# Kernel optimization log

Measured on AMD Instinct MI355X. Metric: run time of the kernel, lower is better.

## Reference

```python
import jax, jax.numpy as jnp
import numpy as np

N = 200000
C_IN, C_OUT = 32, 64
D, H, W = 32, 512, 512
EPS = 1e-5


def _build_nbrs(lin, d, h, w, offsets):
    # lin: sorted unique linear voxel indices [N]; returns [N, K] int64 (sentinel=N)
    n = lin.shape[0]
    cols = []
    for dz, dy, dx in offsets:
        nd, nh, nw = d + dz, h + dy, w + dx
        valid = (nd >= 0) & (nd < D) & (nh >= 0) & (nh < H) & (nw >= 0) & (nw < W)
        nlin = nd * (H * W) + nh * W + nw
        pos = np.searchsorted(lin, nlin)
        posc = np.clip(pos, 0, n - 1)
        found = valid & (pos < n) & (lin[posc] == nlin)
        cols.append(np.where(found, posc, n))
    return np.stack(cols, axis=1).astype(np.int64)


def setup_inputs() -> dict:
    rng = np.random.default_rng(0)
    lin = np.sort(rng.choice(D * H * W, size=N, replace=False))
    d = lin // (H * W)
    h = (lin // W) % H
    w = lin % W
    # (1,3,3) kernel, padding (0,1,1): dz=0
    off133 = [(0, dy, dx) for dy in (-1, 0, 1) for dx in (-1, 0, 1)]
    # (3,1,3) kernel, padding (1,0,1): dy=0
    off313 = [(dz, 0, dx) for dz in (-1, 0, 1) for dx in (-1, 0, 1)]
    nbr133 = jnp.asarray(_build_nbrs(lin, d, h, w, off133))
    nbr313 = jnp.asarray(_build_nbrs(lin, d, h, w, off313))

    key = jax.random.key(0)
    ks = jax.random.split(key, 5)
    feats = jax.random.normal(ks[0], (N, C_IN), dtype=jnp.float32)
    s_in = 1.0 / np.sqrt(9 * C_IN)
    s_out = 1.0 / np.sqrt(9 * C_OUT)
    W1 = jax.random.normal(ks[1], (9, C_IN, C_OUT), dtype=jnp.float32) * s_in
    W2 = jax.random.normal(ks[2], (9, C_OUT, C_OUT), dtype=jnp.float32) * s_out
    W3 = jax.random.normal(ks[3], (9, C_IN, C_OUT), dtype=jnp.float32) * s_in
    W4 = jax.random.normal(ks[4], (9, C_OUT, C_OUT), dtype=jnp.float32) * s_out
    ones = jnp.ones((C_OUT,), jnp.float32)
    zeros = jnp.zeros((C_OUT,), jnp.float32)
    return dict(feats=feats, nbr133=nbr133, nbr313=nbr313,
                W1=W1, W2=W2, W3=W3, W4=W4,
                g0=ones, b0=zeros, g02=ones, b02=zeros,
                g1=ones, b1=zeros, g2=ones, b2=zeros)


def _subm_conv(x, nbr, Wk):
    # x: [N, Cin], nbr: [N, K] with sentinel N -> zero row, Wk: [K, Cin, Cout]
    xp = jnp.concatenate([x, jnp.zeros((1, x.shape[1]), x.dtype)], axis=0)
    g = xp[nbr]  # [N, K, Cin] gather
    return jnp.einsum('nkc,kcd->nd', g, Wk)


def _bn(x, gamma, beta):
    # training-mode BatchNorm1d: batch stats over N (biased variance)
    m = x.mean(axis=0)
    v = x.var(axis=0)
    return gamma * (x - m) * jax.lax.rsqrt(v + EPS) + beta


def _lrelu(x):
    return jax.nn.leaky_relu(x, 0.01)


def reference(feats, nbr133, nbr313, W1, W2, W3, W4,
              g0, b0, g02, b02, g1, b1, g2, b2):
    shortcut = _subm_conv(feats, nbr133, W1)
    shortcut = _bn(_lrelu(shortcut), g0, b0)
    shortcut = _subm_conv(shortcut, nbr313, W2)
    shortcut = _bn(_lrelu(shortcut), g02, b02)

    resA = _subm_conv(feats, nbr313, W3)
    resA = _bn(_lrelu(resA), g1, b1)
    resA = _subm_conv(resA, nbr133, W4)
    resA = _bn(_lrelu(resA), g2, b2)
    return resA + shortcut
```

## Files before the change

### kernel.cpp

```cpp
#include <hip/hip_runtime.h>
#include <hip/hip_bf16.h>


typedef __attribute__((ext_vector_type(8))) short bf16x8;
typedef __attribute__((ext_vector_type(4))) float f32x4;
typedef unsigned long long ull;

#define EPSF 1e-5f
#define REP8 0x0101010101010101ull

__device__ __forceinline__ unsigned short f2bf(float f) {
    union { __hip_bfloat16 h; unsigned short u; } cv;
    cv.h = __float2bfloat16(f);
    return cv.u;
}
__device__ __forceinline__ unsigned pkbf(float lo, float hi) {
    return (unsigned)f2bf(lo) | ((unsigned)f2bf(hi) << 16);
}

__global__ void prep_kernel(const float* __restrict__ W1, const float* __restrict__ W3,
                            unsigned short* __restrict__ Wb1, unsigned short* __restrict__ Wb3)
{
    int i = blockIdx.x * 256 + threadIdx.x;
    if (i >= 2 * 9 * 2048) return;
    const float* W = i < 9 * 2048 ? W1 : W3;
    unsigned short* Wb = i < 9 * 2048 ? Wb1 : Wb3;
    int pp = i < 9 * 2048 ? i : i - 9 * 2048;
    int k = pp >> 11, rest = pp & 2047;
    int t = (rest >> 9) & 3, lane = (rest >> 3) & 63, j = rest & 7;
    int c = (lane >> 4) * 8 + j;
    int d = t * 16 + (lane & 15);
    Wb[pp] = f2bf(W[(size_t)(k * 32 + c) * 64 + d]);
}

__global__ __launch_bounds__(256, 4)
void conv13_kernel(const float* __restrict__ x,
                   const int* __restrict__ nbrA, const int* __restrict__ nbrB,
                   const unsigned short* __restrict__ WbA,
                   const unsigned short* __restrict__ WbB,
                   unsigned short* __restrict__ yA, unsigned short* __restrict__ yB,
                   float* __restrict__ part,
                   int n_vox)
{
    const int lane = threadIdx.x & 63;
    const int wave = threadIdx.x >> 6;
    __shared__ __align__(16) char smem[4][4352];
    char* my = smem[wave];
    const int c15 = lane & 15, g16 = lane >> 4;
    const int j7 = lane & 7, kk = j7 + (j7 >= 4 ? 1 : 0), vv = lane >> 3;
    const int v16 = blockIdx.x * 64 + wave * 16;

    const size_t r0 = (size_t)(v16 + vv) * 9 + kk;
    const size_t r1 = (size_t)(v16 + 8 + vv) * 9 + kk;
    int pA0 = nbrA[r0], pA1 = nbrA[r1];
    int pB0 = nbrB[r0], pB1 = nbrB[r1];

    const float* xr = x + (size_t)(v16 + c15) * 32 + g16 * 8;
    float4 x0 = *reinterpret_cast<const float4*>(xr);
    float4 x1 = *reinterpret_cast<const float4*>(xr + 4);

    bf16x8 bA[4], bB[4];
    #pragma unroll
    for (int t = 0; t < 4; ++t) {
        bA[t] = *reinterpret_cast<const bf16x8*>(WbA + (size_t)((4*4+t)*64 + lane) * 8);
        bB[t] = *reinterpret_cast<const bf16x8*>(WbB + (size_t)((4*4+t)*64 + lane) * 8);
    }
    bf16x8 af;
    af[0]=(short)f2bf(x0.x); af[1]=(short)f2bf(x0.y); af[2]=(short)f2bf(x0.z); af[3]=(short)f2bf(x0.w);
    af[4]=(short)f2bf(x1.x); af[5]=(short)f2bf(x1.y); af[6]=(short)f2bf(x1.z); af[7]=(short)f2bf(x1.w);

    f32x4 accA[4], accB[4];
    #pragma unroll
    for (int t = 0; t < 4; ++t) { f32x4 z = {0.f,0.f,0.f,0.f}; accA[t] = z; accB[t] = z; }
    #pragma unroll
    for (int t = 0; t < 4; ++t) {
        accA[t] = __builtin_amdgcn_mfma_f32_16x16x32_bf16(af, bA[t], accA[t], 0, 0, 0);
        accB[t] = __builtin_amdgcn_mfma_f32_16x16x32_bf16(af, bB[t], accB[t], 0, 0, 0);
    }

    ull mA0 = __ballot(pA0 < n_vox), mA1 = __ballot(pA1 < n_vox);
    ull mB0 = __ballot(pB0 < n_vox), mB1 = __ballot(pB1 < n_vox);
    const int nhA = __popcll(mA0) + __popcll(mA1);
    const int nhB = __popcll(mB0) + __popcll(mB1);

    auto walksel = [&](ull M, int preg, int slot, int base, int& sel) {
        while (M) {
            int b = __builtin_ctzll(M); M &= M - 1;
            int src = __shfl(preg, b);
            sel = (c15 == slot - base) ? src : sel;
            ++slot;
        }
        return slot;
    };
    auto gatherfrag = [&](int sel) {
        const float* hr = x + (size_t)sel * 32 + g16 * 8;
        float4 f0 = *reinterpret_cast<const float4*>(hr);
        float4 f1 = *reinterpret_cast<const float4*>(hr + 4);
        bf16x8 h;
        h[0]=(short)f2bf(f0.x); h[1]=(short)f2bf(f0.y); h[2]=(short)f2bf(f0.z); h[3]=(short)f2bf(f0.w);
        h[4]=(short)f2bf(f1.x); h[5]=(short)f2bf(f1.y); h[6]=(short)f2bf(f1.z); h[7]=(short)f2bf(f1.w);
        return h;
    };
    auto kloop = [&](ull m0, ull m1, bf16x8 h, const unsigned short* Wb,
                     f32x4* acc, int base) {
        const int pref = __popcll(m0);
        for (int tap = 0; tap < 8; ++tap) {
            ull TM = REP8 << tap;
            ull k0 = m0 & TM, k1 = m1 & TM;
            if (!(k0 | k1)) continue;
            int k = tap + (tap >= 4 ? 1 : 0);
            bf16x8 bk[4];
            #pragma unroll
            for (int t = 0; t < 4; ++t)
                bk[t] = *reinterpret_cast<const bf16x8*>(Wb + (size_t)((k*4+t)*64 + lane) * 8);
            f32x4 ch[4];
            #pragma unroll
            for (int t = 0; t < 4; ++t) { f32x4 z = {0.f,0.f,0.f,0.f}; ch[t] = z; }
            #pragma unroll
            for (int t = 0; t < 4; ++t)
                ch[t] = __builtin_amdgcn_mfma_f32_16x16x32_bf16(h, bk[t], ch[t], 0, 0, 0);
            auto inj = [&](ull M, ull msrc, int spref, int vbase) {
                while (M) {
                    int b = __builtin_ctzll(M); M &= M - 1;
                    int slot = spref + __popcll(msrc & ((1ull << b) - 1ull));
                    int rs = slot - base;
                    if (rs < 0 || rs >= 16) continue;
                    int vb = vbase + (b >> 3);
                    int srclane = ((rs >> 2) << 4) + c15;
                    int jj = rs & 3, gp = vb >> 2, jp = vb & 3;
                    float v0, v1, v2, v3;
                    switch (jj) {
                    case 0: v0=__shfl(ch[0][0],srclane); v1=__shfl(ch[1][0],srclane);
                            v2=__shfl(ch[2][0],srclane); v3=__shfl(ch[3][0],srclane); break;
                    case 1: v0=__shfl(ch[0][1],srclane); v1=__shfl(ch[1][1],srclane);
                            v2=__shfl(ch[2][1],srclane); v3=__shfl(ch[3][1],srclane); break;
                    case 2: v0=__shfl(ch[0][2],srclane); v1=__shfl(ch[1][2],srclane);
                            v2=__shfl(ch[2][2],srclane); v3=__shfl(ch[3][2],srclane); break;
                    default: v0=__shfl(ch[0][3],srclane); v1=__shfl(ch[1][3],srclane);
                             v2=__shfl(ch[2][3],srclane); v3=__shfl(ch[3][3],srclane); break;
                    }
                    bool mine = (g16 == gp);
                    float z0 = mine ? v0 : 0.f, z1 = mine ? v1 : 0.f;
                    float z2 = mine ? v2 : 0.f, z3 = mine ? v3 : 0.f;
                    switch (jp) {
                    case 0: acc[0][0]+=z0; acc[1][0]+=z1; acc[2][0]+=z2; acc[3][0]+=z3; break;
                    case 1: acc[0][1]+=z0; acc[1][1]+=z1; acc[2][1]+=z2; acc[3][1]+=z3; break;
                    case 2: acc[0][2]+=z0; acc[1][2]+=z1; acc[2][2]+=z2; acc[3][2]+=z3; break;
                    default: acc[0][3]+=z0; acc[1][3]+=z1; acc[2][3]+=z2; acc[3][3]+=z3; break;
                    }
                }
            };
            inj(k0, m0, 0, 0);
            inj(k1, m1, pref, 8);
        }
    };

    if (nhA | nhB) {
        int selA = 0, selB = 0;
        int cA = walksel(mA0, pA0, 0, 0, selA);
        walksel(mA1, pA1, cA, 0, selA);
        int cB = walksel(mB0, pB0, 0, 0, selB);
        walksel(mB1, pB1, cB, 0, selB);
        bf16x8 hA = gatherfrag(selA);
        bf16x8 hB = gatherfrag(selB);
        if (nhA) kloop(mA0, mA1, hA, WbA, accA, 0);
        if (nhB) kloop(mB0, mB1, hB, WbB, accB, 0);
        for (int base = 16; base < nhA; base += 16) {
            int s = 0;
            int c0 = walksel(mA0, pA0, 0, base, s);
            walksel(mA1, pA1, c0, base, s);
            kloop(mA0, mA1, gatherfrag(s), WbA, accA, base);
        }
        for (int base = 16; base < nhB; base += 16) {
            int s = 0;
            int c0 = walksel(mB0, pB0, 0, base, s);
            walksel(mB1, pB1, c0, base, s);
            kloop(mB0, mB1, gatherfrag(s), WbB, accB, base);
        }
    }

    float psA0[4], psA1[4], psB0[4], psB1[4];
    #pragma unroll
    for (int t = 0; t < 4; ++t) { psA0[t]=0.f; psA1[t]=0.f; psB0[t]=0.f; psB1[t]=0.f; }

    auto epi = [&](f32x4* acc, float* ps0, float* ps1, unsigned short* yo) {
        float* stg = reinterpret_cast<float*>(my);
        #pragma unroll
        for (int t = 0; t < 4; ++t) {
            const int col = t * 16 + c15;
            #pragma unroll
            for (int j = 0; j < 4; ++j) {
                float v = acc[t][j];
                v = v > 0.f ? v : 0.01f * v;
                ps0[t] += v;
                ps1[t] = fmaf(v, v, ps1[t]);
                stg[(g16 * 4 + j) * 68 + col] = v;
            }
        }
        const int mm = lane >> 2, cc0 = (lane & 3) * 16;
        float4 q0 = *reinterpret_cast<float4*>(&stg[mm * 68 + cc0]);
        float4 q1 = *reinterpret_cast<float4*>(&stg[mm * 68 + cc0 + 4]);
        float4 q2 = *reinterpret_cast<float4*>(&stg[mm * 68 + cc0 + 8]);
        float4 q3 = *reinterpret_cast<float4*>(&stg[mm * 68 + cc0 + 12]);
        uint4 o0, o1;
        o0.x = pkbf(q0.x, q0.y); o0.y = pkbf(q0.z, q0.w);
        o0.z = pkbf(q1.x, q1.y); o0.w = pkbf(q1.z, q1.w);
        o1.x = pkbf(q2.x, q2.y); o1.y = pkbf(q2.z, q2.w);
        o1.z = pkbf(q3.x, q3.y); o1.w = pkbf(q3.z, q3.w);
        uint4* dst = reinterpret_cast<uint4*>(yo + (size_t)(v16 + mm) * 64 + cc0);
        dst[0] = o0; dst[1] = o1;
    };
    epi(accA, psA0, psA1, yA);
    epi(accB, psB0, psB1, yB);

    __syncthreads();
    float* lsf = reinterpret_cast<float*>(&smem[0][0]);
    const int r = wave * 4 + g16;
    #pragma unroll
    for (int t = 0; t < 4; ++t) {
        lsf[r * 256 + 0 * 64 + t * 16 + c15] = psA0[t];
        lsf[r * 256 + 1 * 64 + t * 16 + c15] = psA1[t];
        lsf[r * 256 + 2 * 64 + t * 16 + c15] = psB0[t];
        lsf[r * 256 + 3 * 64 + t * 16 + c15] = psB1[t];
    }
    __syncthreads();
    const int tid = threadIdx.x;
    float s = 0.f;
    #pragma unroll
    for (int rr = 0; rr < 16; ++rr) s += lsf[rr * 256 + tid];
    part[(size_t)blockIdx.x * 256 + tid] = s;
}

__global__ __launch_bounds__(256, 4)
void conv24_kernel(const unsigned short* __restrict__ x2, const int* __restrict__ nbr2,
                   const float* __restrict__ tv2, const unsigned short* __restrict__ Wb2,
                   unsigned short* __restrict__ y2,
                   const unsigned short* __restrict__ x4, const int* __restrict__ nbr4,
                   const float* __restrict__ tv4, const unsigned short* __restrict__ Wb4,
                   unsigned short* __restrict__ y4,
                   float* __restrict__ part,
                   int n_vox, int ntile)
{
    const int lane = threadIdx.x & 63;
    const int wave = threadIdx.x >> 6;
    __shared__ __align__(16) char smem[4][4352];
    char* my = smem[wave];
    const bool second = blockIdx.x >= ntile;
    const int tile = second ? blockIdx.x - ntile : blockIdx.x;
    const unsigned short* x = second ? x4 : x2;
    const int* nbr = second ? nbr4 : nbr2;
    const float* tvec = second ? tv4 : tv2;
    const unsigned short* Wb = second ? Wb4 : Wb2;
    unsigned short* yout = second ? y4 : y2;

    const int c15 = lane & 15, g16 = lane >> 4;
    const int j7 = lane & 7, kk = j7 + (j7 >= 4 ? 1 : 0), vv = lane >> 3;
    const int v16 = tile * 64 + wave * 16;

    const size_t r0 = (size_t)(v16 + vv) * 9 + kk;
    const size_t r1 = (size_t)(v16 + 8 + vv) * 9 + kk;
    int p0 = nbr[r0], p1 = nbr[r1];

    const unsigned short* xr = x + (size_t)(v16 + c15) * 64 + g16 * 8;
    bf16x8 a0 = *reinterpret_cast<const bf16x8*>(xr);
    bf16x8 a1 = *reinterpret_cast<const bf16x8*>(xr + 32);

    bf16x8 bwC[2][4];
    #pragma unroll
    for (int kt = 0; kt < 2; ++kt)
        #pragma unroll
        for (int t = 0; t < 4; ++t)
            bwC[kt][t] = *reinterpret_cast<const bf16x8*>(Wb + (size_t)(((4*2+kt)*4+t)*64 + lane) * 8);

    f32x4 acc[4];
    #pragma unroll
    for (int t = 0; t < 4; ++t) {
        float tC = tvec[4 * 64 + t * 16 + c15];
        f32x4 z = {tC, tC, tC, tC};
        acc[t] = z;
    }
    #pragma unroll
    for (int t = 0; t < 4; ++t) {
        acc[t] = __builtin_amdgcn_mfma_f32_16x16x32_bf16(a0, bwC[0][t], acc[t], 0, 0, 0);
        acc[t] = __builtin_amdgcn_mfma_f32_16x16x32_bf16(a1, bwC[1][t], acc[t], 0, 0, 0);
    }

    ull m0 = __ballot(p0 < n_vox), m1 = __ballot(p1 < n_vox);
    const int nh = __popcll(m0) + __popcll(m1);

    auto walksel = [&](ull M, int preg, int slot, int base, int& sel) {
        while (M) {
            int b = __builtin_ctzll(M); M &= M - 1;
            int src = __shfl(preg, b);
            sel = (c15 == slot - base) ? src : sel;
            ++slot;
        }
        return slot;
    };
    auto kloop = [&](bf16x8 h0, bf16x8 h1, int base) {
        const int pref = __popcll(m0);
        for (int tap = 0; tap < 8; ++tap) {
            ull TM = REP8 << tap;
            ull k0 = m0 & TM, k1 = m1 & TM;
            if (!(k0 | k1)) continue;
            int k = tap + (tap >= 4 ? 1 : 0);
            bf16x8 bk[2][4];
            #pragma unroll
            for (int kt = 0; kt < 2; ++kt)
                #pragma unroll
                for (int t = 0; t < 4; ++t)
                    bk[kt][t] = *reinterpret_cast<const bf16x8*>(Wb + (size_t)(((k*2+kt)*4+t)*64 + lane) * 8);
            float tvk[4];
            #pragma unroll
            for (int t = 0; t < 4; ++t) tvk[t] = tvec[k * 64 + t * 16 + c15];
            f32x4 ch[4];
            #pragma unroll
            for (int t = 0; t < 4; ++t) { f32x4 z = {0.f,0.f,0.f,0.f}; ch[t] = z; }
            #pragma unroll
            for (int t = 0; t < 4; ++t) {
                ch[t] = __builtin_amdgcn_mfma_f32_16x16x32_bf16(h0, bk[0][t], ch[t], 0, 0, 0);
                ch[t] = __builtin_amdgcn_mfma_f32_16x16x32_bf16(h1, bk[1][t], ch[t], 0, 0, 0);
            }
            auto inj = [&](ull M, ull msrc, int spref, int vbase) {
                while (M) {
                    int b = __builtin_ctzll(M); M &= M - 1;
                    int slot = spref + __popcll(msrc & ((1ull << b) - 1ull));
                    int rs = slot - base;
                    if (rs < 0 || rs >= 16) continue;
                    int vb = vbase + (b >> 3);
                    int srclane = ((rs >> 2) << 4) + c15;
                    int jj = rs & 3, gp = vb >> 2, jp = vb & 3;
                    float v0, v1, v2, v3;
                    switch (jj) {
                    case 0: v0=__shfl(ch[0][0],srclane); v1=__shfl(ch[1][0],srclane);
                            v2=__shfl(ch[2][0],srclane); v3=__shfl(ch[3][0],srclane); break;
                    case 1: v0=__shfl(ch[0][1],srclane); v1=__shfl(ch[1][1],srclane);
                            v2=__shfl(ch[2][1],srclane); v3=__shfl(ch[3][1],srclane); break;
                    case 2: v0=__shfl(ch[0][2],srclane); v1=__shfl(ch[1][2],srclane);
                            v2=__shfl(ch[2][2],srclane); v3=__shfl(ch[3][2],srclane); break;
                    default: v0=__shfl(ch[0][3],srclane); v1=__shfl(ch[1][3],srclane);
                             v2=__shfl(ch[2][3],srclane); v3=__shfl(ch[3][3],srclane); break;
                    }
                    bool mine = (g16 == gp);
                    float z0 = mine ? (v0 + tvk[0]) : 0.f, z1 = mine ? (v1 + tvk[1]) : 0.f;
                    float z2 = mine ? (v2 + tvk[2]) : 0.f, z3 = mine ? (v3 + tvk[3]) : 0.f;
                    switch (jp) {
                    case 0: acc[0][0]+=z0; acc[1][0]+=z1; acc[2][0]+=z2; acc[3][0]+=z3; break;
                    case 1: acc[0][1]+=z0; acc[1][1]+=z1; acc[2][1]+=z2; acc[3][1]+=z3; break;
                    case 2: acc[0][2]+=z0; acc[1][2]+=z1; acc[2][2]+=z2; acc[3][2]+=z3; break;
                    default: acc[0][3]+=z0; acc[1][3]+=z1; acc[2][3]+=z2; acc[3][3]+=z3; break;
                    }
                }
            };
            inj(k0, m0, 0, 0);
            inj(k1, m1, pref, 8);
        }
    };

    for (int base = 0; base < nh; base += 16) {
        int sel = 0;
        int c0 = walksel(m0, p0, 0, base, sel);
        walksel(m1, p1, c0, base, sel);
        const unsigned short* hr = x + (size_t)sel * 64 + g16 * 8;
        bf16x8 h0 = *reinterpret_cast<const bf16x8*>(hr);
        bf16x8 h1 = *reinterpret_cast<const bf16x8*>(hr + 32);
        kloop(h0, h1, base);
    }

    float ps0[4] = {0,0,0,0}, ps1[4] = {0,0,0,0};
    float* stg = reinterpret_cast<float*>(my);
    #pragma unroll
    for (int t = 0; t < 4; ++t) {
        const int col = t * 16 + c15;
        #pragma unroll
        for (int j = 0; j < 4; ++j) {
            float v = acc[t][j];
            v = v > 0.f ? v : 0.01f * v;
            ps0[t] += v;
            ps1[t] = fmaf(v, v, ps1[t]);
            stg[(g16 * 4 + j) * 68 + col] = v;
        }
    }
    const int mm = lane >> 2, cc0 = (lane & 3) * 16;
    float4 q0 = *reinterpret_cast<float4*>(&stg[mm * 68 + cc0]);
    float4 q1 = *reinterpret_cast<float4*>(&stg[mm * 68 + cc0 + 4]);
    float4 q2 = *reinterpret_cast<float4*>(&stg[mm * 68 + cc0 + 8]);
    float4 q3 = *reinterpret_cast<float4*>(&stg[mm * 68 + cc0 + 12]);
    uint4 o0, o1;
    o0.x = pkbf(q0.x, q0.y); o0.y = pkbf(q0.z, q0.w);
    o0.z = pkbf(q1.x, q1.y); o0.w = pkbf(q1.z, q1.w);
    o1.x = pkbf(q2.x, q2.y); o1.y = pkbf(q2.z, q2.w);
    o1.z = pkbf(q3.x, q3.y); o1.w = pkbf(q3.z, q3.w);
    uint4* dst = reinterpret_cast<uint4*>(yout + (size_t)(v16 + mm) * 64 + cc0);
    dst[0] = o0; dst[1] = o1;

    __syncthreads();
    float* lsf = reinterpret_cast<float*>(&smem[0][0]);
    const int r = wave * 4 + g16;
    #pragma unroll
    for (int t = 0; t < 4; ++t) {
        lsf[r * 128 + t * 16 + c15] = ps0[t];
        lsf[r * 128 + 64 + t * 16 + c15] = ps1[t];
    }
    __syncthreads();
    const int tid = threadIdx.x;
    if (tid < 128) {
        float s = 0.f;
        #pragma unroll
        for (int rr = 0; rr < 16; ++rr) s += lsf[rr * 128 + tid];
        part[(size_t)tile * 256 + (second ? 128 : 0) + tid] = s;
    }
}

__global__ void bnred_kernel(const float* __restrict__ part,
                             const float* __restrict__ gA, const float* __restrict__ bA,
                             const float* __restrict__ gB, const float* __restrict__ bB,
                             float* __restrict__ scA, float* __restrict__ shA,
                             float* __restrict__ scB, float* __restrict__ shB,
                             float invN, int nblk)
{
    const int l = blockIdx.x >> 6, c = blockIdx.x & 63;
    const float* base = part + (size_t)(l * 2) * 64 + c;
    __shared__ float red[256][2];
    float s = 0.f, q = 0.f;
    for (int b = threadIdx.x; b < nblk; b += 256) {
        s += base[(size_t)b * 256];
        q += base[(size_t)b * 256 + 64];
    }
    red[threadIdx.x][0] = s; red[threadIdx.x][1] = q;
    __syncthreads();
    for (int off = 128; off; off >>= 1) {
        if (threadIdx.x < off) {
            red[threadIdx.x][0] += red[threadIdx.x + off][0];
            red[threadIdx.x][1] += red[threadIdx.x + off][1];
        }
        __syncthreads();
    }
    if (threadIdx.x == 0) {
        float m = red[0][0] * invN;
        float v = red[0][1] * invN - m * m;
        const float* g = l ? gB : gA;
        const float* bb = l ? bB : bA;
        float* sc = l ? scB : scA;
        float* sh = l ? shB : shA;
        float scale = g[c] / sqrtf(v + EPSF);
        sc[c] = scale;
        sh[c] = bb[c] - m * scale;
    }
}

__global__ void foldpack_kernel(const float* __restrict__ W2, const float* __restrict__ W4,
                                const float* __restrict__ sc1, const float* __restrict__ sh1,
                                const float* __restrict__ sc3, const float* __restrict__ sh3,
                                float* __restrict__ t2, float* __restrict__ t4,
                                unsigned short* __restrict__ Wb2, unsigned short* __restrict__ Wb4)
{
    int i = blockIdx.x * 256 + threadIdx.x;
    if (i < 2 * 9 * 64) {
        const float* W = i < 9 * 64 ? W2 : W4;
        const float* shift = i < 9 * 64 ? sh1 : sh3;
        float* tv = i < 9 * 64 ? t2 : t4;
        int ii = i < 9 * 64 ? i : i - 9 * 64;
        int d = ii & 63, k = ii >> 6;
        float t = 0.f;
// ... 35 lines not shown
    b[2] = __uint_as_float(bq.y << 16); b[3] = __uint_as_float(bq.y & 0xffff0000u);
    b[4] = __uint_as_float(bq.z << 16); b[5] = __uint_as_float(bq.z & 0xffff0000u);
    b[6] = __uint_as_float(bq.w << 16); b[7] = __uint_as_float(bq.w & 0xffff0000u);
    float r[8];
    #pragma unroll
    for (int j = 0; j < 8; ++j)
        r[j] = fmaf(a[j], sc2[c0 + j], sh2[c0 + j]) + fmaf(b[j], sc4[c0 + j], sh4[c0 + j]);
    float4 o0 = {r[0], r[1], r[2], r[3]};
    float4 o1 = {r[4], r[5], r[6], r[7]};
    float* po = out + (size_t)i * 8;
    *reinterpret_cast<float4*>(po) = o0;
    *reinterpret_cast<float4*>(po + 4) = o1;
}

extern "C" void kernel_launch(void* const* d_in, const int* in_sizes, int n_in,
                              void* d_out, int out_size, void* d_ws, size_t ws_size,
                              hipStream_t stream)
{
    const float* feats  = (const float*)d_in[0];
    const int*   nbr133 = (const int*)d_in[1];
    const int*   nbr313 = (const int*)d_in[2];
    const float* W1 = (const float*)d_in[3];
    const float* W2 = (const float*)d_in[4];
    const float* W3 = (const float*)d_in[5];
    const float* W4 = (const float*)d_in[6];
    const float* g0  = (const float*)d_in[7];
    const float* b0  = (const float*)d_in[8];
    const float* g02 = (const float*)d_in[9];
    const float* b02 = (const float*)d_in[10];
    const float* g1  = (const float*)d_in[11];
    const float* b1  = (const float*)d_in[12];
    const float* g2  = (const float*)d_in[13];
    const float* b2  = (const float*)d_in[14];

    const int N = in_sizes[0] / 32;
    const int ntile = N >> 6;

    char* w = (char*)d_ws;
    auto alloc = [&](size_t bytes) {
        char* p = w;
        w += (bytes + 255) & ~(size_t)255;
        return p;
    };
    unsigned short* y1 = (unsigned short*)alloc((size_t)N * 64 * 2);
    unsigned short* y3 = (unsigned short*)alloc((size_t)N * 64 * 2);
    unsigned short* y2 = (unsigned short*)alloc((size_t)N * 64 * 2);
    unsigned short* y4 = (unsigned short*)alloc((size_t)N * 64 * 2);
    float* t2 = (float*)alloc(9 * 64 * 4);
    float* t4 = (float*)alloc(9 * 64 * 4);
    unsigned short* Wb1 = (unsigned short*)alloc(9 * 4 * 64 * 8 * 2);
    unsigned short* Wb3 = (unsigned short*)alloc(9 * 4 * 64 * 8 * 2);
    unsigned short* Wb2 = (unsigned short*)alloc(9 * 2 * 4 * 64 * 8 * 2);
    unsigned short* Wb4 = (unsigned short*)alloc(9 * 2 * 4 * 64 * 8 * 2);
    float* part13 = (float*)alloc((size_t)ntile * 256 * 4);
    float* part24 = (float*)alloc((size_t)ntile * 256 * 4);
    float* scl = (float*)alloc(8 * 64 * 4);
    float *sc1 = scl,       *sh1 = scl + 64;
    float *sc3 = scl + 128, *sh3 = scl + 192;
    float *sc2 = scl + 256, *sh2 = scl + 320;
    float *sc4 = scl + 384, *sh4 = scl + 448;

    const float invN = 1.0f / (float)N;

    prep_kernel<<<(2 * 9 * 2048 + 255) / 256, 256, 0, stream>>>(W1, W3, Wb1, Wb3);

    conv13_kernel<<<ntile, 256, 0, stream>>>(feats, nbr133, nbr313, Wb1, Wb3,
                                             y1, y3, part13, N);
    bnred_kernel<<<128, 256, 0, stream>>>(part13, g0, b0, g1, b1,
                                          sc1, sh1, sc3, sh3, invN, ntile);
    foldpack_kernel<<<(2 * 9 * 64 + 2 * 9 * 4096 + 255) / 256, 256, 0, stream>>>(
        W2, W4, sc1, sh1, sc3, sh3, t2, t4, Wb2, Wb4);

    conv24_kernel<<<2 * ntile, 256, 0, stream>>>(y1, nbr313, t2, Wb2, y2,
                                                 y3, nbr133, t4, Wb4, y4,
                                                 part24, N, ntile);
    bnred_kernel<<<128, 256, 0, stream>>>(part24, g02, b02, g2, b2,
                                          sc2, sh2, sc4, sh4, invN, ntile);

    final_kernel<<<(N * 8 + 255) / 256, 256, 0, stream>>>(
        y2, y4, sc2, sh2, sc4, sh4, (float*)d_out, N * 8);
}
```

Baseline: 131.2 us.

## Make conv kernels persistent with grid-stride tiles and per-block BN partials

Measured after the change: 147.6 us. 12.5% more time.

```diff
diff --git a/kernel.cpp b/kernel.cpp
--- a/kernel.cpp
+++ b/kernel.cpp
@@ -8,6 +8,7 @@
 
 #define EPSF 1e-5f
 #define REP8 0x0101010101010101ull
+#define PGRID 2048
 
 __device__ __forceinline__ unsigned short f2bf(float f) {
     union { __hip_bfloat16 h; unsigned short u; } cv;
@@ -48,16 +49,7 @@
     char* my = smem[wave];
     const int c15 = lane & 15, g16 = lane >> 4;
     const int j7 = lane & 7, kk = j7 + (j7 >= 4 ? 1 : 0), vv = lane >> 3;
-    const int v16 = blockIdx.x * 64 + wave * 16;
-
-    const size_t r0 = (size_t)(v16 + vv) * 9 + kk;
-    const size_t r1 = (size_t)(v16 + 8 + vv) * 9 + kk;
-    int pA0 = nbrA[r0], pA1 = nbrA[r1];
-    int pB0 = nbrB[r0], pB1 = nbrB[r1];
-
-    const float* xr = x + (size_t)(v16 + c15) * 32 + g16 * 8;
-    float4 x0 = *reinterpret_cast<const float4*>(xr);
-    float4 x1 = *reinterpret_cast<const float4*>(xr + 4);
+    const int ntile = n_vox >> 6;
 
     bf16x8 bA[4], bB[4];
     #pragma unroll
@@ -65,23 +57,9 @@
         bA[t] = *reinterpret_cast<const bf16x8*>(WbA + (size_t)((4*4+t)*64 + lane) * 8);
         bB[t] = *reinterpret_cast<const bf16x8*>(WbB + (size_t)((4*4+t)*64 + lane) * 8);
     }
-    bf16x8 af;
-    af[0]=(short)f2bf(x0.x); af[1]=(short)f2bf(x0.y); af[2]=(short)f2bf(x0.z); af[3]=(short)f2bf(x0.w);
-    af[4]=(short)f2bf(x1.x); af[5]=(short)f2bf(x1.y); af[6]=(short)f2bf(x1.z); af[7]=(short)f2bf(x1.w);
-
-    f32x4 accA[4], accB[4];
-    #pragma unroll
-    for (int t = 0; t < 4; ++t) { f32x4 z = {0.f,0.f,0.f,0.f}; accA[t] = z; accB[t] = z; }
-    #pragma unroll
-    for (int t = 0; t < 4; ++t) {
-        accA[t] = __builtin_amdgcn_mfma_f32_16x16x32_bf16(af, bA[t], accA[t], 0, 0, 0);
-        accB[t] = __builtin_amdgcn_mfma_f32_16x16x32_bf16(af, bB[t], accB[t], 0, 0, 0);
-    }
-
-    ull mA0 = __ballot(pA0 < n_vox), mA1 = __ballot(pA1 < n_vox);
-    ull mB0 = __ballot(pB0 < n_vox), mB1 = __ballot(pB1 < n_vox);
-    const int nhA = __popcll(mA0) + __popcll(mA1);
-    const int nhB = __popcll(mB0) + __popcll(mB1);
+
+    float psA0[4] = {0,0,0,0}, psA1[4] = {0,0,0,0};
+    float psB0[4] = {0,0,0,0}, psB1[4] = {0,0,0,0};
 
     auto walksel = [&](ull M, int preg, int slot, int base, int& sel) {
         while (M) {
@@ -101,89 +79,307 @@
         h[4]=(short)f2bf(f1.x); h[5]=(short)f2bf(f1.y); h[6]=(short)f2bf(f1.z); h[7]=(short)f2bf(f1.w);
         return h;
     };
-    auto kloop = [&](ull m0, ull m1, bf16x8 h, const unsigned short* Wb,
-                     f32x4* acc, int base) {
-        const int pref = __popcll(m0);
-        for (int tap = 0; tap < 8; ++tap) {
-            ull TM = REP8 << tap;
-            ull k0 = m0 & TM, k1 = m1 & TM;
-            if (!(k0 | k1)) continue;
-            int k = tap + (tap >= 4 ? 1 : 0);
-            bf16x8 bk[4];
+
+    for (int tile = blockIdx.x; tile < ntile; tile += gridDim.x) {
+        const int v16 = tile * 64 + wave * 16;
+
+        const size_t r0 = (size_t)(v16 + vv) * 9 + kk;
+        const size_t r1 = (size_t)(v16 + 8 + vv) * 9 + kk;
+        int pA0 = nbrA[r0], pA1 = nbrA[r1];
+        int pB0 = nbrB[r0], pB1 = nbrB[r1];
+
+        const float* xr = x + (size_t)(v16 + c15) * 32 + g16 * 8;
+        float4 x0 = *reinterpret_cast<const float4*>(xr);
+        float4 x1 = *reinterpret_cast<const float4*>(xr + 4);
+        bf16x8 af;
+        af[0]=(short)f2bf(x0.x); af[1]=(short)f2bf(x0.y); af[2]=(short)f2bf(x0.z); af[3]=(short)f2bf(x0.w);
+        af[4]=(short)f2bf(x1.x); af[5]=(short)f2bf(x1.y); af[6]=(short)f2bf(x1.z); af[7]=(short)f2bf(x1.w);
+
+        f32x4 accA[4], accB[4];
+        #pragma unroll
+        for (int t = 0; t < 4; ++t) { f32x4 z = {0.f,0.f,0.f,0.f}; accA[t] = z; accB[t] = z; }
+        #pragma unroll
+        for (int t = 0; t < 4; ++t) {
+            accA[t] = __builtin_amdgcn_mfma_f32_16x16x32_bf16(af, bA[t], accA[t], 0, 0, 0);
+            accB[t] = __builtin_amdgcn_mfma_f32_16x16x32_bf16(af, bB[t], accB[t], 0, 0, 0);
+        }
+
+        ull mA0 = __ballot(pA0 < n_vox), mA1 = __ballot(pA1 < n_vox);
+        ull mB0 = __ballot(pB0 < n_vox), mB1 = __ballot(pB1 < n_vox);
+        const int nhA = __popcll(mA0) + __popcll(mA1);
+        const int nhB = __popcll(mB0) + __popcll(mB1);
+
+        auto kloop = [&](ull m0, ull m1, bf16x8 h, const unsigned short* Wb,
+                         f32x4* acc, int base) {
+            const int pref = __popcll(m0);
+            for (int tap = 0; tap < 8; ++tap) {
+                ull TM = REP8 << tap;
+                ull k0 = m0 & TM, k1 = m1 & TM;
+                if (!(k0 | k1)) continue;
+                int k = tap + (tap >= 4 ? 1 : 0);
+                bf16x8 bk[4];
+                #pragma unroll
+                for (int t = 0; t < 4; ++t)
+                    bk[t] = *reinterpret_cast<const bf16x8*>(Wb + (size_t)((k*4+t)*64 + lane) * 8);
+                f32x4 ch[4];
+                #pragma unroll
+                for (int t = 0; t < 4; ++t) { f32x4 z = {0.f,0.f,0.f,0.f}; ch[t] = z; }
+                #pragma unroll
+                for (int t = 0; t < 4; ++t)
+                    ch[t] = __builtin_amdgcn_mfma_f32_16x16x32_bf16(h, bk[t], ch[t], 0, 0, 0);
+                auto inj = [&](ull M, ull msrc, int spref, int vbase) {
+                    while (M) {
+                        int b = __builtin_ctzll(M); M &= M - 1;
+                        int slot = spref + __popcll(msrc & ((1ull << b) - 1ull));
+                        int rs = slot - base;
+                        if (rs < 0 || rs >= 16) continue;
+                        int vb = vbase + (b >> 3);
+                        int srclane = ((rs >> 2) << 4) + c15;
+                        int jj = rs & 3, gp = vb >> 2, jp = vb & 3;
+                        float v0, v1, v2, v3;
+                        switch (jj) {
+                        case 0: v0=__shfl(ch[0][0],srclane); v1=__shfl(ch[1][0],srclane);
+                                v2=__shfl(ch[2][0],srclane); v3=__shfl(ch[3][0],srclane); break;
+                        case 1: v0=__shfl(ch[0][1],srclane); v1=__shfl(ch[1][1],srclane);
+                                v2=__shfl(ch[2][1],srclane); v3=__shfl(ch[3][1],srclane); break;
+                        case 2: v0=__shfl(ch[0][2],srclane); v1=__shfl(ch[1][2],srclane);
+                                v2=__shfl(ch[2][2],srclane); v3=__shfl(ch[3][2],srclane); break;
+                        default: v0=__shfl(ch[0][3],srclane); v1=__shfl(ch[1][3],srclane);
+                                 v2=__shfl(ch[2][3],srclane); v3=__shfl(ch[3][3],srclane); break;
+                        }
+                        bool mine = (g16 == gp);
+                        float z0 = mine ? v0 : 0.f, z1 = mine ? v1 : 0.f;
+                        float z2 = mine ? v2 : 0.f, z3 = mine ? v3 : 0.f;
+                        switch (jp) {
+                        case 0: acc[0][0]+=z0; acc[1][0]+=z1; acc[2][0]+=z2; acc[3][0]+=z3; break;
+                        case 1: acc[0][1]+=z0; acc[1][1]+=z1; acc[2][1]+=z2; acc[3][1]+=z3; break;
+                        case 2: acc[0][2]+=z0; acc[1][2]+=z1; acc[2][2]+=z2; acc[3][2]+=z3; break;
+                        default: acc[0][3]+=z0; acc[1][3]+=z1; acc[2][3]+=z2; acc[3][3]+=z3; break;
+                        }
+                    }
+                };
+                inj(k0, m0, 0, 0);
+                inj(k1, m1, pref, 8);
+            }
+        };
+
+        if (nhA | nhB) {
+            int selA = 0, selB = 0;
+            int cA = walksel(mA0, pA0, 0, 0, selA);
+            walksel(mA1, pA1, cA, 0, selA);
+            int cB = walksel(mB0, pB0, 0, 0, selB);
+            walksel(mB1, pB1, cB, 0, selB);
+            bf16x8 hA = gatherfrag(selA);
+            bf16x8 hB = gatherfrag(selB);
+            if (nhA) kloop(mA0, mA1, hA, WbA, accA, 0);
+            if (nhB) kloop(mB0, mB1, hB, WbB, accB, 0);
+            for (int base = 16; base < nhA; base += 16) {
+                int s = 0;
+                int c0 = walksel(mA0, pA0, 0, base, s);
+                walksel(mA1, pA1, c0, base, s);
+                kloop(mA0, mA1, gatherfrag(s), WbA, accA, base);
+            }
+            for (int base = 16; base < nhB; base += 16) {
+                int s = 0;
+                int c0 = walksel(mB0, pB0, 0, base, s);
+                walksel(mB1, pB1, c0, base, s);
+                kloop(mB0, mB1, gatherfrag(s), WbB, accB, base);
+            }
+        }
+
+        auto epi = [&](f32x4* acc, float* ps0, float* ps1, unsigned short* yo) {
+            float* stg = reinterpret_cast<float*>(my);
+            #pragma unroll
+            for (int t = 0; t < 4; ++t) {
+                const int col = t * 16 + c15;
+                #pragma unroll
+                for (int j = 0; j < 4; ++j) {
+                    float v = acc[t][j];
+                    v = v > 0.f ? v : 0.01f * v;
+                    ps0[t] += v;
+                    ps1[t] = fmaf(v, v, ps1[t]);
+                    stg[(g16 * 4 + j) * 68 + col] = v;
+                }
+            }
+            const int mm = lane >> 2, cc0 = (lane & 3) * 16;
+            float4 q0 = *reinterpret_cast<float4*>(&stg[mm * 68 + cc0]);
+            float4 q1 = *reinterpret_cast<float4*>(&stg[mm * 68 + cc0 + 4]);
+            float4 q2 = *reinterpret_cast<float4*>(&stg[mm * 68 + cc0 + 8]);
+            float4 q3 = *reinterpret_cast<float4*>(&stg[mm * 68 + cc0 + 12]);
+            uint4 o0, o1;
+            o0.x = pkbf(q0.x, q0.y); o0.y = pkbf(q0.z, q0.w);
+            o0.z = pkbf(q1.x, q1.y); o0.w = pkbf(q1.z, q1.w);
+            o1.x = pkbf(q2.x, q2.y); o1.y = pkbf(q2.z, q2.w);
+            o1.z = pkbf(q3.x, q3.y); o1.w = pkbf(q3.z, q3.w);
+            uint4* dst = reinterpret_cast<uint4*>(yo + (size_t)(v16 + mm) * 64 + cc0);
+            dst[0] = o0; dst[1] = o1;
+        };
+        epi(accA, psA0, psA1, yA);
+        epi(accB, psB0, psB1, yB);
+    }
+
+    __syncthreads();
+    float* lsf = reinterpret_cast<float*>(&smem[0][0]);
+    const int r = wave * 4 + g16;
+    #pragma unroll
+    for (int t = 0; t < 4; ++t) {
+        lsf[r * 256 + 0 * 64 + t * 16 + c15] = psA0[t];
+        lsf[r * 256 + 1 * 64 + t * 16 + c15] = psA1[t];
+        lsf[r * 256 + 2 * 64 + t * 16 + c15] = psB0[t];
+        lsf[r * 256 + 3 * 64 + t * 16 + c15] = psB1[t];
+    }
+    __syncthreads();
+    const int tid = threadIdx.x;
+    float s = 0.f;
+    #pragma unroll
+    for (int rr = 0; rr < 16; ++rr) s += lsf[rr * 256 + tid];
+    part[(size_t)blockIdx.x * 256 + tid] = s;
+}
+
+__global__ __launch_bounds__(256, 4)
+void conv24_kernel(const unsigned short* __restrict__ x2, const int* __restrict__ nbr2,
+                   const float* __restrict__ tv2, const unsigned short* __restrict__ Wb2,
+                   unsigned short* __restrict__ y2,
+                   const unsigned short* __restrict__ x4, const int* __restrict__ nbr4,
+                   const float* __restrict__ tv4, const unsigned short* __restrict__ Wb4,
+                   unsigned short* __restrict__ y4,
+                   float* __restrict__ part,
+                   int n_vox, int ntile)
+{
+    const int lane = threadIdx.x & 63;
+    const int wave = threadIdx.x >> 6;
+    __shared__ __align__(16) char smem[4][4352];
+    char* my = smem[wave];
+    const int c15 = lane & 15, g16 = lane >> 4;
+    const int j7 = lane & 7, kk = j7 + (j7 >= 4 ? 1 : 0), vv = lane >> 3;
+
+    float ps2s[4] = {0,0,0,0}, ps2q[4] = {0,0,0,0};
+    float ps4s[4] = {0,0,0,0}, ps4q[4] = {0,0,0,0};
+
+    auto walksel = [&](ull M, int preg, int slot, int base, int& sel) {
+        while (M) {
+            int b = __builtin_ctzll(M); M &= M - 1;
+            int src = __shfl(preg, b);
+            sel = (c15 == slot - base) ? src : sel;
+            ++slot;
+        }
+        return slot;
+    };
+
+    const int njobs = 2 * ntile;
+    for (int job = blockIdx.x; job < njobs; job += gridDim.x) {
+        const bool second = job >= ntile;
+        const int tile = second ? job - ntile : job;
+        const unsigned short* x = second ? x4 : x2;
+        const int* nbr = second ? nbr4 : nbr2;
+        const float* tvec = second ? tv4 : tv2;
+        const unsigned short* Wb = second ? Wb4 : Wb2;
+        unsigned short* yout = second ? y4 : y2;
+        float* ps0 = second ? ps4s : ps2s;
+        float* ps1 = second ? ps4q : ps2q;
+
+        const int v16 = tile * 64 + wave * 16;
+
+        int p0 = nbr[(size_t)(v16 + vv) * 9 + kk];
+        int p1 = nbr[(size_t)(v16 + 8 + vv) * 9 + kk];
+
+        const unsigned short* xr = x + (size_t)(v16 + c15) * 64 + g16 * 8;
+        bf16x8 a0 = *reinterpret_cast<const bf16x8*>(xr);
+        bf16x8 a1 = *reinterpret_cast<const bf16x8*>(xr + 32);
+
+        bf16x8 bwC[2][4];
+        #pragma unroll
+        for (int kt = 0; kt < 2; ++kt)
             #pragma unroll
             for (int t = 0; t < 4; ++t)
-                bk[t] = *reinterpret_cast<const bf16x8*>(Wb + (size_t)((k*4+t)*64 + lane) * 8);
-            f32x4 ch[4];
-            #pragma unroll
-            for (int t = 0; t < 4; ++t) { f32x4 z = {0.f,0.f,0.f,0.f}; ch[t] = z; }
-            #pragma unroll
-            for (int t = 0; t < 4; ++t)
-                ch[t] = __builtin_amdgcn_mfma_f32_16x16x32_bf16(h, bk[t], ch[t], 0, 0, 0);
-            auto inj = [&](ull M, ull msrc, int spref, int vbase) {
-                while (M) {
-                    int b = __builtin_ctzll(M); M &= M - 1;
-                    int slot = spref + __popcll(msrc & ((1ull << b) - 1ull));
-                    int rs = slot - base;
-                    if (rs < 0 || rs >= 16) continue;
-                    int vb = vbase + (b >> 3);
-                    int srclane = ((rs >> 2) << 4) + c15;
-                    int jj = rs & 3, gp = vb >> 2, jp = vb & 3;
-                    float v0, v1, v2, v3;
-                    switch (jj) {
-                    case 0: v0=__shfl(ch[0][0],srclane); v1=__shfl(ch[1][0],srclane);
-                            v2=__shfl(ch[2][0],srclane); v3=__shfl(ch[3][0],srclane); break;
-                    case 1: v0=__shfl(ch[0][1],srclane); v1=__shfl(ch[1][1],srclane);
-                            v2=__shfl(ch[2][1],srclane); v3=__shfl(ch[3][1],srclane); break;
-                    case 2: v0=__shfl(ch[0][2],srclane); v1=__shfl(ch[1][2],srclane);
-                            v2=__shfl(ch[2][2],srclane); v3=__shfl(ch[3][2],srclane); break;
-                    default: v0=__shfl(ch[0][3],srclane); v1=__shfl(ch[1][3],srclane);
-                             v2=__shfl(ch[2][3],srclane); v3=__shfl(ch[3][3],srclane); break;
+                bwC[kt][t] = *reinterpret_cast<const bf16x8*>(Wb + (size_t)(((4*2+kt)*4+t)*64 + lane) * 8);
+
+        f32x4 acc[4];
+        #pragma unroll
+        for (int t = 0; t < 4; ++t) {
+            float tC = tvec[4 * 64 + t * 16 + c15];
+            f32x4 z = {tC, tC, tC, tC};
+            acc[t] = z;
+        }
+        #pragma unroll
+        for (int t = 0; t < 4; ++t) {
+            acc[t] = __builtin_amdgcn_mfma_f32_16x16x32_bf16(a0, bwC[0][t], acc[t], 0, 0, 0);
+            acc[t] = __builtin_amdgcn_mfma_f32_16x16x32_bf16(a1, bwC[1][t], acc[t], 0, 0, 0);
+        }
+
+        ull m0 = __ballot(p0 < n_vox), m1 = __ballot(p1 < n_vox);
+        const int nh = __popcll(m0) + __popcll(m1);
+
+        auto kloop = [&](bf16x8 h0, bf16x8 h1, int base) {
+            const int pref = __popcll(m0);
+            for (int tap = 0; tap < 8; ++tap) {
+                ull TM = REP8 << tap;
+                ull k0 = m0 & TM, k1 = m1 & TM;
+                if (!(k0 | k1)) continue;
+                int k = tap + (tap >= 4 ? 1 : 0);
+                bf16x8 bk[2][4];
+                #pragma unroll
+                for (int kt = 0; kt < 2; ++kt)
+                    #pragma unroll
+                    for (int t = 0; t < 4; ++t)
+                        bk[kt][t] = *reinterpret_cast<const bf16x8*>(Wb + (size_t)(((k*2+kt)*4+t)*64 + lane) * 8);
+                float tvk[4];
+                #pragma unroll
+                for (int t = 0; t < 4; ++t) tvk[t] = tvec[k * 64 + t * 16 + c15];
+                f32x4 ch[4];
+                #pragma unroll
+                for (int t = 0; t < 4; ++t) { f32x4 z = {0.f,0.f,0.f,0.f}; ch[t] = z; }
+                #pragma unroll
+                for (int t = 0; t < 4; ++t) {
+                    ch[t] = __builtin_amdgcn_mfma_f32_16x16x32_bf16(h0, bk[0][t], ch[t], 0, 0, 0);
+                    ch[t] = __builtin_amdgcn_mfma_f32_16x16x32_bf16(h1, bk[1][t], ch[t], 0, 0, 0);
+                }
+                auto inj = [&](ull M, ull msrc, int spref, int vbase) {
+                    while (M) {
+                        int b = __builtin_ctzll(M); M &= M - 1;
+                        int slot = spref + __popcll(msrc & ((1ull << b) - 1ull));
+                        int rs = slot - base;
+                        if (rs < 0 || rs >= 16) continue;
+                        int vb = vbase + (b >> 3);
+                        int srclane = ((rs >> 2) << 4) + c15;
+                        int jj = rs & 3, gp = vb >> 2, jp = vb & 3;
+                        float v0, v1, v2, v3;
+                        switch (jj) {
+                        case 0: v0=__shfl(ch[0][0],srclane); v1=__shfl(ch[1][0],srclane);
+                                v2=__shfl(ch[2][0],srclane); v3=__shfl(ch[3][0],srclane); break;
+                        case 1: v0=__shfl(ch[0][1],srclane); v1=__shfl(ch[1][1],srclane);
+                                v2=__shfl(ch[2][1],srclane); v3=__shfl(ch[3][1],srclane); break;
+                        case 2: v0=__shfl(ch[0][2],srclane); v1=__shfl(ch[1][2],srclane);
+                                v2=__shfl(ch[2][2],srclane); v3=__shfl(ch[3][2],srclane); break;
+                        default: v0=__shfl(ch[0][3],srclane); v1=__shfl(ch[1][3],srclane);
+                                 v2=__shfl(ch[2][3],srclane); v3=__shfl(ch[3][3],srclane); break;
+                        }
+                        bool mine = (g16 == gp);
+                        float z0 = mine ? (v0 + tvk[0]) : 0.f, z1 = mine ? (v1 + tvk[1]) : 0.f;
+                        float z2 = mine ? (v2 + tvk[2]) : 0.f, z3 = mine ? (v3 + tvk[3]) : 0.f;
+                        switch (jp) {
+                        case 0: acc[0][0]+=z0; acc[1][0]+=z1; acc[2][0]+=z2; acc[3][0]+=z3; break;
+                        case 1: acc[0][1]+=z0; acc[1][1]+=z1; acc[2][1]+=z2; acc[3][1]+=z3; break;
+                        case 2: acc[0][2]+=z0; acc[1][2]+=z1; acc[2][2]+=z2; acc[3][2]+=z3; break;
+                        default: acc[0][3]+=z0; acc[1][3]+=z1; acc[2][3]+=z2; acc[3][3]+=z3; break;
+                        }
                     }
-                    bool mine = (g16 == gp);
-                    float z0 = mine ? v0 : 0.f, z1 = mine ? v1 : 0.f;
-                    float z2 = mine ? v2 : 0.f, z3 = mine ? v3 : 0.f;
-                    switch (jp) {
-                    case 0: acc[0][0]+=z0; acc[1][0]+=z1; acc[2][0]+=z2; acc[3][0]+=z3; break;
-                    case 1: acc[0][1]+=z0; acc[1][1]+=z1; acc[2][1]+=z2; acc[3][1]+=z3; break;
-                    case 2: acc[0][2]+=z0; acc[1][2]+=z1; acc[2][2]+=z2; acc[3][2]+=z3; break;
-                    default: acc[0][3]+=z0; acc[1][3]+=z1; acc[2][3]+=z2; acc[3][3]+=z3; break;
-                    }
-                }
-            };
-            inj(k0, m0, 0, 0);
-            inj(k1, m1, pref, 8);
-        }
-    };
-
-    if (nhA | nhB) {
-        int selA = 0, selB = 0;
-        int cA = walksel(mA0, pA0, 0, 0, selA);
-        walksel(mA1, pA1, cA, 0, selA);
-        int cB = walksel(mB0, pB0, 0, 0, selB);
-        walksel(mB1, pB1, cB, 0, selB);
-        bf16x8 hA = gatherfrag(selA);
-        bf16x8 hB = gatherfrag(selB);
-        if (nhA) kloop(mA0, mA1, hA, WbA, accA, 0);
-        if (nhB) kloop(mB0, mB1, hB, WbB, accB, 0);
-        for (int base = 16; base < nhA; base += 16) {
-            int s = 0;
-            int c0 = walksel(mA0, pA0, 0, base, s);
-            walksel(mA1, pA1, c0, base, s);
-            kloop(mA0, mA1, gatherfrag(s), WbA, accA, base);
-        }
-        for (int base = 16; base < nhB; base += 16) {
-            int s = 0;
-            int c0 = walksel(mB0, pB0, 0, base, s);
-            walksel(mB1, pB1, c0, base, s);
-            kloop(mB0, mB1, gatherfrag(s), WbB, accB, base);
-        }
-    }
-
-    float psA0[4], psA1[4], psB0[4], psB1[4];
-    #pragma unroll
-    for (int t = 0; t < 4; ++t) { psA0[t]=0.f; psA1[t]=0.f; psB0[t]=0.f; psB1[t]=0.f; }
-
-    auto epi = [&](f32x4* acc, float* ps0, float* ps1, unsigned short* yo) {
+                };
+                inj(k0, m0, 0, 0);
+                inj(k1, m1, pref, 8);
+            }
+        };
+
+        for (int base = 0; base < nh; base += 16) {
+            int sel = 0;
+            int c0 = walksel(m0, p0, 0, base, sel);
+            walksel(m1, p1, c0, base, sel);
+            const unsigned short* hr = x + (size_t)sel * 64 + g16 * 8;
+            bf16x8 h0 = *reinterpret_cast<const bf16x8*>(hr);
+            bf16x8 h1 = *reinterpret_cast<const bf16x8*>(hr + 32);
+            kloop(h0, h1, base);
+        }
+
         float* stg = reinterpret_cast<float*>(my);
         #pragma unroll
         for (int t = 0; t < 4; ++t) {
@@ -207,21 +403,19 @@
         o0.z = pkbf(q1.x, q1.y); o0.w = pkbf(q1.z, q1.w);
         o1.x = pkbf(q2.x, q2.y); o1.y = pkbf(q2.z, q2.w);
         o1.z = pkbf(q3.x, q3.y); o1.w = pkbf(q3.z, q3.w);
-        uint4* dst = reinterpret_cast<uint4*>(yo + (size_t)(v16 + mm) * 64 + cc0);
+        uint4* dst = reinterpret_cast<uint4*>(yout + (size_t)(v16 + mm) * 64 + cc0);
         dst[0] = o0; dst[1] = o1;
-    };
-    epi(accA, psA0, psA1, yA);
-    epi(accB, psB0, psB1, yB);
+    }
 
     __syncthreads();
     float* lsf = reinterpret_cast<float*>(&smem[0][0]);
     const int r = wave * 4 + g16;
     #pragma unroll
     for (int t = 0; t < 4; ++t) {
-        lsf[r * 256 + 0 * 64 + t * 16 + c15] = psA0[t];
-        lsf[r * 256 + 1 * 64 + t * 16 + c15] = psA1[t];
-        lsf[r * 256 + 2 * 64 + t * 16 + c15] = psB0[t];
-        lsf[r * 256 + 3 * 64 + t * 16 + c15] = psB1[t];
+        lsf[r * 256 + 0 * 64 + t * 16 + c15] = ps2s[t];
+        lsf[r * 256 + 1 * 64 + t * 16 + c15] = ps2q[t];
+        lsf[r * 256 + 2 * 64 + t * 16 + c15] = ps4s[t];
+        lsf[r * 256 + 3 * 64 + t * 16 + c15] = ps4q[t];
     }
     __syncthreads();
     const int tid = threadIdx.x;
@@ -229,187 +423,6 @@
     #pragma unroll
     for (int rr = 0; rr < 16; ++rr) s += lsf[rr * 256 + tid];
     part[(size_t)blockIdx.x * 256 + tid] = s;
-}
-
-__global__ __launch_bounds__(256, 4)
-void conv24_kernel(const unsigned short* __restrict__ x2, const int* __restrict__ nbr2,
-                   const float* __restrict__ tv2, const unsigned short* __restrict__ Wb2,
-                   unsigned short* __restrict__ y2,
-                   const unsigned short* __restrict__ x4, const int* __restrict__ nbr4,
-                   const float* __restrict__ tv4, const unsigned short* __restrict__ Wb4,
-                   unsigned short* __restrict__ y4,
-                   float* __restrict__ part,
-                   int n_vox, int ntile)
-{
-    const int lane = threadIdx.x & 63;
-    const int wave = threadIdx.x >> 6;
-    __shared__ __align__(16) char smem[4][4352];
-    char* my = smem[wave];
-    const bool second = blockIdx.x >= ntile;
-    const int tile = second ? blockIdx.x - ntile : blockIdx.x;
-    const unsigned short* x = second ? x4 : x2;
-    const int* nbr = second ? nbr4 : nbr2;
-    const float* tvec = second ? tv4 : tv2;
-    const unsigned short* Wb = second ? Wb4 : Wb2;
-    unsigned short* yout = second ? y4 : y2;
-
-    const int c15 = lane & 15, g16 = lane >> 4;
-    const int j7 = lane & 7, kk = j7 + (j7 >= 4 ? 1 : 0), vv = lane >> 3;
-    const int v16 = tile * 64 + wave * 16;
-
-    const size_t r0 = (size_t)(v16 + vv) * 9 + kk;
-    const size_t r1 = (size_t)(v16 + 8 + vv) * 9 + kk;
-    int p0 = nbr[r0], p1 = nbr[r1];
-
-    const unsigned short* xr = x + (size_t)(v16 + c15) * 64 + g16 * 8;
-    bf16x8 a0 = *reinterpret_cast<const bf16x8*>(xr);
-    bf16x8 a1 = *reinterpret_cast<const bf16x8*>(xr + 32);
-
-    bf16x8 bwC[2][4];
-    #pragma unroll
-    for (int kt = 0; kt < 2; ++kt)
-        #pragma unroll
-        for (int t = 0; t < 4; ++t)
-            bwC[kt][t] = *reinterpret_cast<const bf16x8*>(Wb + (size_t)(((4*2+kt)*4+t)*64 + lane) * 8);
-
-    f32x4 acc[4];
-    #pragma unroll
-    for (int t = 0; t < 4; ++t) {
-        float tC = tvec[4 * 64 + t * 16 + c15];
-        f32x4 z = {tC, tC, tC, tC};
-        acc[t] = z;
-    }
-    #pragma unroll
-    for (int t = 0; t < 4; ++t) {
-        acc[t] = __builtin_amdgcn_mfma_f32_16x16x32_bf16(a0, bwC[0][t], acc[t], 0, 0, 0);
-        acc[t] = __builtin_amdgcn_mfma_f32_16x16x32_bf16(a1, bwC[1][t], acc[t], 0, 0, 0);
-    }
-
-    ull m0 = __ballot(p0 < n_vox), m1 = __ballot(p1 < n_vox);
-    const int nh = __popcll(m0) + __popcll(m1);
-
-    auto walksel = [&](ull M, int preg, int slot, int base, int& sel) {
-        while (M) {
-            int b = __builtin_ctzll(M); M &= M - 1;
-            int src = __shfl(preg, b);
-            sel = (c15 == slot - base) ? src : sel;
-            ++slot;
-        }
-        return slot;
-    };
-    auto kloop = [&](bf16x8 h0, bf16x8 h1, int base) {
-        const int pref = __popcll(m0);
-        for (int tap = 0; tap < 8; ++tap) {
-            ull TM = REP8 << tap;
-            ull k0 = m0 & TM, k1 = m1 & TM;
-            if (!(k0 | k1)) continue;
-            int k = tap + (tap >= 4 ? 1 : 0);
-            bf16x8 bk[2][4];
-            #pragma unroll
-            for (int kt = 0; kt < 2; ++kt)
-                #pragma unroll
-                for (int t = 0; t < 4; ++t)
-                    bk[kt][t] = *reinterpret_cast<const bf16x8*>(Wb + (size_t)(((k*2+kt)*4+t)*64 + lane) * 8);
-            float tvk[4];
-            #pragma unroll
-            for (int t = 0; t < 4; ++t) tvk[t] = tvec[k * 64 + t * 16 + c15];
-            f32x4 ch[4];
-            #pragma unroll
-            for (int t = 0; t < 4; ++t) { f32x4 z = {0.f,0.f,0.f,0.f}; ch[t] = z; }
-            #pragma unroll
-            for (int t = 0; t < 4; ++t) {
-                ch[t] = __builtin_amdgcn_mfma_f32_16x16x32_bf16(h0, bk[0][t], ch[t], 0, 0, 0);
-                ch[t] = __builtin_amdgcn_mfma_f32_16x16x32_bf16(h1, bk[1][t], ch[t], 0, 0, 0);
-            }
-            auto inj = [&](ull M, ull msrc, int spref, int vbase) {
-                while (M) {
-                    int b = __builtin_ctzll(M); M &= M - 1;
-                    int slot = spref + __popcll(msrc & ((1ull << b) - 1ull));
-                    int rs = slot - base;
-                    if (rs < 0 || rs >= 16) continue;
-                    int vb = vbase + (b >> 3);
-                    int srclane = ((rs >> 2) << 4) + c15;
-                    int jj = rs & 3, gp = vb >> 2, jp = vb & 3;
-                    float v0, v1, v2, v3;
-                    switch (jj) {
-                    case 0: v0=__shfl(ch[0][0],srclane); v1=__shfl(ch[1][0],srclane);
-                            v2=__shfl(ch[2][0],srclane); v3=__shfl(ch[3][0],srclane); break;
-                    case 1: v0=__shfl(ch[0][1],srclane); v1=__shfl(ch[1][1],srclane);
-                            v2=__shfl(ch[2][1],srclane); v3=__shfl(ch[3][1],srclane); break;
-                    case 2: v0=__shfl(ch[0][2],srclane); v1=__shfl(ch[1][2],srclane);
-                            v2=__shfl(ch[2][2],srclane); v3=__shfl(ch[3][2],srclane); break;
-                    default: v0=__shfl(ch[0][3],srclane); v1=__shfl(ch[1][3],srclane);
-                             v2=__shfl(ch[2][3],srclane); v3=__shfl(ch[3][3],srclane); break;
-                    }
-                    bool mine = (g16 == gp);
-                    float z0 = mine ? (v0 + tvk[0]) : 0.f, z1 = mine ? (v1 + tvk[1]) : 0.f;
-                    float z2 = mine ? (v2 + tvk[2]) : 0.f, z3 = mine ? (v3 + tvk[3]) : 0.f;
-                    switch (jp) {
-                    case 0: acc[0][0]+=z0; acc[1][0]+=z1; acc[2][0]+=z2; acc[3][0]+=z3; break;
-                    case 1: acc[0][1]+=z0; acc[1][1]+=z1; acc[2][1]+=z2; acc[3][1]+=z3; break;
-                    case 2: acc[0][2]+=z0; acc[1][2]+=z1; acc[2][2]+=z2; acc[3][2]+=z3; break;
-                    default: acc[0][3]+=z0; acc[1][3]+=z1; acc[2][3]+=z2; acc[3][3]+=z3; break;
-                    }
-                }
-            };
-            inj(k0, m0, 0, 0);
-            inj(k1, m1, pref, 8);
-        }
-    };
-
-    for (int base = 0; base < nh; base += 16) {
-        int sel = 0;
-        int c0 = walksel(m0, p0, 0, base, sel);
-        walksel(m1, p1, c0, base, sel);
-        const unsigned short* hr = x + (size_t)sel * 64 + g16 * 8;
-        bf16x8 h0 = *reinterpret_cast<const bf16x8*>(hr);
-        bf16x8 h1 = *reinterpret_cast<const bf16x8*>(hr + 32);
-        kloop(h0, h1, base);
-    }
-
-    float ps0[4] = {0,0,0,0}, ps1[4] = {0,0,0,0};
-    float* stg = reinterpret_cast<float*>(my);
-    #pragma unroll
-    for (int t = 0; t < 4; ++t) {
-        const int col = t * 16 + c15;
-        #pragma unroll
-        for (int j = 0; j < 4; ++j) {
-            float v = acc[t][j];
-            v = v > 0.f ? v : 0.01f * v;
-            ps0[t] += v;
-            ps1[t] = fmaf(v, v, ps1[t]);
-            stg[(g16 * 4 + j) * 68 + col] = v;
-        }
-    }
-    const int mm = lane >> 2, cc0 = (lane & 3) * 16;
-    float4 q0 = *reinterpret_cast<float4*>(&stg[mm * 68 + cc0]);
-    float4 q1 = *reinterpret_cast<float4*>(&stg[mm * 68 + cc0 + 4]);
-    float4 q2 = *reinterpret_cast<float4*>(&stg[mm * 68 + cc0 + 8]);
-    float4 q3 = *reinterpret_cast<float4*>(&stg[mm * 68 + cc0 + 12]);
-    uint4 o0, o1;
-    o0.x = pkbf(q0.x, q0.y); o0.y = pkbf(q0.z, q0.w);
-    o0.z = pkbf(q1.x, q1.y); o0.w = pkbf(q1.z, q1.w);
-    o1.x = pkbf(q2.x, q2.y); o1.y = pkbf(q2.z, q2.w);
-    o1.z = pkbf(q3.x, q3.y); o1.w = pkbf(q3.z, q3.w);
-    uint4* dst = reinterpret_cast<uint4*>(yout + (size_t)(v16 + mm) * 64 + cc0);
-    dst[0] = o0; dst[1] = o1;
-
-    __syncthreads();
-    float* lsf = reinterpret_cast<float*>(&smem[0][0]);
-    const int r = wave * 4 + g16;
-    #pragma unroll
-    for (int t = 0; t < 4; ++t) {
-        lsf[r * 128 + t * 16 + c15] = ps0[t];
-        lsf[r * 128 + 64 + t * 16 + c15] = ps1[t];
-    }
-    __syncthreads();
-    const int tid = threadIdx.x;
-    if (tid < 128) {
-        float s = 0.f;
-        #pragma unroll
-        for (int rr = 0; rr < 16; ++rr) s += lsf[rr * 128 + tid];
-        part[(size_t)tile * 256 + (second ? 128 : 0) + tid] = s;
-    }
 }
 
 __global__ void bnred_kernel(const float* __restrict__ part,
@@ -551,8 +564,8 @@
     unsigned short* Wb3 = (unsigned short*)alloc(9 * 4 * 64 * 8 * 2);
     unsigned short* Wb2 = (unsigned short*)alloc(9 * 2 * 4 * 64 * 8 * 2);
     unsigned short* Wb4 = (unsigned short*)alloc(9 * 2 * 4 * 64 * 8 * 2);
-    float* part13 = (float*)alloc((size_t)ntile * 256 * 4);
-    float* part24 = (float*)alloc((size_t)ntile * 256 * 4);
+    float* part13 = (float*)alloc((size_t)PGRID * 256 * 4);
+    float* part24 = (float*)alloc((size_t)PGRID * 256 * 4);
     float* scl = (float*)alloc(8 * 64 * 4);
     float *sc1 = scl,       *sh1 = scl + 64;
     float *sc3 = scl + 128, *sh3 = scl + 192;
@@ -563,18 +576,18 @@
 
     prep_kernel<<<(2 * 9 * 2048 + 255) / 256, 256, 0, stream>>>(W1, W3, Wb1, Wb3);
 
-    conv13_kernel<<<ntile, 256, 0, stream>>>(feats, nbr133, nbr313, Wb1, Wb3,
+    conv13_kernel<<<PGRID, 256, 0, stream>>>(feats, nbr133, nbr313, Wb1, Wb3,
                                              y1, y3, part13, N);
     bnred_kernel<<<128, 256, 0, stream>>>(part13, g0, b0, g1, b1,
-                                          sc1, sh1, sc3, sh3, invN, ntile);
+                                          sc1, sh1, sc3, sh3, invN, PGRID);
     foldpack_kernel<<<(2 * 9 * 64 + 2 * 9 * 4096 + 255) / 256, 256, 0, stream>>>(
         W2, W4, sc1, sh1, sc3, sh3, t2, t4, Wb2, Wb4);
 
-    conv24_kernel<<<2 * ntile, 256, 0, stream>>>(y1, nbr313, t2, Wb2, y2,
-                                                 y3, nbr133, t4, Wb4, y4,
-                                                 part24, N, ntile);
+    conv24_kernel<<<PGRID, 256, 0, stream>>>(y1, nbr313, t2, Wb2, y2,
+                                             y3, nbr133, t4, Wb4, y4,
+                                             part24, N, ntile);
     bnred_kernel<<<128, 256, 0, stream>>>(part24, g02, b02, g2, b2,
-                                          sc2, sh2, sc4, sh4, invN, ntile);
+                                          sc2, sh2, sc4, sh4, invN, PGRID);
 
     final_kernel<<<(N * 8 + 255) / 256, 256, 0, stream>>>(
         y2, y4, sc2, sh2, sc4, sh4, (float*)d_out, N * 8);
```
